# Optimization experiments

Hardware: AMD Instinct MI355X
Metric: run time of the kernel (lower is better)

The kernel has to match this reference:

```python
import jax, jax.numpy as jnp
import numpy as np

H = 16
D_MODEL = 1024
D_K = D_MODEL // H
B, S = 8, 1024


def setup_inputs() -> dict:
    key = jax.random.key(0)
    ks = jax.random.split(key, 11)
    scale = 1.0 / np.sqrt(D_MODEL)
    inp = {
        "query": jax.random.normal(ks[0], (B, S, D_MODEL), jnp.float32),
        "key_": jax.random.normal(ks[1], (B, S, D_MODEL), jnp.float32),
        "value": jax.random.normal(ks[2], (B, S, D_MODEL), jnp.float32),
        "w_q": jax.random.normal(ks[3], (D_MODEL, D_MODEL), jnp.float32) * scale,
        "b_q": jnp.zeros((D_MODEL,), jnp.float32),
        "w_k": jax.random.normal(ks[4], (D_MODEL, D_MODEL), jnp.float32) * scale,
        "b_k": jnp.zeros((D_MODEL,), jnp.float32),
        "w_v": jax.random.normal(ks[5], (D_MODEL, D_MODEL), jnp.float32) * scale,
        "b_v": jnp.zeros((D_MODEL,), jnp.float32),
        "w_o": jax.random.normal(ks[6], (D_MODEL, D_MODEL), jnp.float32) * scale,
        "b_o": jnp.zeros((D_MODEL,), jnp.float32),
    }
    return inp


def reference(query, key_, value, w_q, b_q, w_k, b_k, w_v, b_v, w_o, b_o):
    # Linear projections (torch Linear: x @ W.T + b), then split heads: [B,S,D] -> [B,H,S,d_k]
    def proj(x, w, b):
        y = jnp.einsum("bsd,ed->bse", x, w) + b
        return y.reshape(B, S, H, D_K).transpose(0, 2, 1, 3)

    q = proj(query, w_q, b_q)
    k = proj(key_, w_k, b_k)
    v = proj(value, w_v, b_v)

    # Scaled dot-product attention (mask=None, dropout p=0 -> identity)
    scores = jnp.einsum("bhqd,bhkd->bhqk", q, k) / jnp.sqrt(jnp.float32(D_K))
    attn = jax.nn.softmax(scores, axis=-1)
    ctx = jnp.einsum("bhqk,bhkd->bhqd", attn, v)  # [B,H,S,d_k]

    # Merge heads and final output projection
    ctx = ctx.transpose(0, 2, 1, 3).reshape(B, S, D_MODEL)
    return jnp.einsum("bsd,ed->bse", ctx, w_o) + b_o
```

## Files before the change

### kernel.cpp

```cpp
#include <hip/hip_runtime.h>
#include <hip/hip_bf16.h>

#define NH 16
#define DK 64
#define BB 8
#define SS 1024
#define DM 1024
#define MTOT (BB * SS)

typedef float f4v __attribute__((ext_vector_type(4)));
typedef float f16v __attribute__((ext_vector_type(16)));
typedef short s16v8 __attribute__((ext_vector_type(8)));
typedef unsigned short u16v4 __attribute__((ext_vector_type(4)));
typedef unsigned short u16v8 __attribute__((ext_vector_type(8)));

#define EXP2F(x) __builtin_amdgcn_exp2f(x)
#define WAIT_VM2() __builtin_amdgcn_s_waitcnt(0x0F72)
#define WAIT_VM0() __builtin_amdgcn_s_waitcnt(0x0F70)

__device__ __forceinline__ unsigned short f2bf(float x) {
    unsigned int u = __float_as_uint(x);
    u += 0x7FFFu + ((u >> 16) & 1u);
    return (unsigned short)(u >> 16);
}

__device__ __forceinline__ unsigned int packbf2(float lo, float hi) {
    return ((unsigned int)f2bf(hi) << 16) | f2bf(lo);
}

__device__ __forceinline__ void gload16(const void* g, void* l) {
    __builtin_amdgcn_global_load_lds(
        (const __attribute__((address_space(1))) void*)g,
        (__attribute__((address_space(3))) void*)l, 16, 0, 0);
}

struct Src7 { const float* p[7]; };

__global__ __launch_bounds__(256) void cvt_all(Src7 sp, unsigned short* __restrict__ dst) {
    const size_t e = ((size_t)blockIdx.x * 256 + threadIdx.x) * 8;
    const int unit = (int)(e >> 20);
    int t; size_t base;
    if (unit < 8)       { t = 0; base = 0; }
    else if (unit < 16) { t = 1; base = (size_t)8 << 20; }
    else if (unit < 24) { t = 2; base = (size_t)16 << 20; }
    else                { t = 3 + (unit - 24); base = (size_t)unit << 20; }
    const float* s = sp.p[t] + (e - base);
    f4v a = *(const f4v*)s;
    f4v b = *(const f4v*)(s + 4);
    u16v8 o;
    o[0] = f2bf(a[0]); o[1] = f2bf(a[1]); o[2] = f2bf(a[2]); o[3] = f2bf(a[3]);
    o[4] = f2bf(b[0]); o[5] = f2bf(b[1]); o[6] = f2bf(b[2]); o[7] = f2bf(b[3]);
    *(u16v8*)(dst + e) = o;
}

struct QkvArgs {
    const unsigned short* X[3];
    const unsigned short* W[3];
    const float* bias[3];
    unsigned short* Y[3];
};

__global__ __launch_bounds__(256) void gemm_qkv(QkvArgs a) {
    __shared__ unsigned short As[128 * 32];
    __shared__ unsigned short Bs[128 * 32];
    const int z = blockIdx.z;
    const unsigned short* X = a.X[z];
    const unsigned short* W = a.W[z];
    const float* bias = a.bias[z];
    unsigned short* Y = a.Y[z];

    const int tid = threadIdx.x;
    const int wv = tid >> 6, l = tid & 63;
    const int lq = l & 15, g = l >> 4;
    const int wr = wv >> 1, wc = wv & 1;
    const int m0 = blockIdx.x * 128, n0 = blockIdx.y * 128;

    f4v acc[4][4];
#pragma unroll
    for (int i = 0; i < 4; ++i)
#pragma unroll
        for (int j = 0; j < 4; ++j) acc[i][j] = (f4v){0.f, 0.f, 0.f, 0.f};

    for (int kt = 0; kt < DM / 32; ++kt) {
        const int k0 = kt * 32;
        __syncthreads();
#pragma unroll
        for (int p = 0; p < 2; ++p) {
            const int u = p * 256 + tid;
            const int row = u >> 2, kc = u & 3;
            gload16(X + (size_t)(m0 + row) * DM + k0 + kc * 8, As + (size_t)u * 8);
            gload16(W + (size_t)(n0 + row) * DM + k0 + kc * 8, Bs + (size_t)u * 8);
        }
        __syncthreads();

        s16v8 av[4], bv[4];
#pragma unroll
        for (int i = 0; i < 4; ++i)
            av[i] = *(const s16v8*)(As + (wr * 64 + i * 16 + lq) * 32 + g * 8);
#pragma unroll
        for (int j = 0; j < 4; ++j)
            bv[j] = *(const s16v8*)(Bs + (wc * 64 + j * 16 + lq) * 32 + g * 8);
#pragma unroll
        for (int i = 0; i < 4; ++i)
#pragma unroll
            for (int j = 0; j < 4; ++j)
                acc[i][j] = __builtin_amdgcn_mfma_f32_16x16x32_bf16(av[i], bv[j], acc[i][j], 0, 0, 0);
    }

#pragma unroll
    for (int j = 0; j < 4; ++j) {
        const int col = n0 + wc * 64 + j * 16 + lq;
        const float bvl = bias[col];
#pragma unroll
        for (int i = 0; i < 4; ++i) {
            const int row0 = m0 + wr * 64 + i * 16 + g * 4;
            if (z < 2) {
#pragma unroll
                for (int r = 0; r < 4; ++r) {
                    const int row = row0 + r;
                    const int b_ = row >> 10, s_ = row & (SS - 1);
                    const int h_ = col >> 6, d_ = col & (DK - 1);
                    Y[((size_t)(b_ * NH + h_) * SS + s_) * DK + d_] = f2bf(acc[i][j][r] + bvl);
                }
            } else {
                const int b_ = row0 >> 10, s0_ = row0 & (SS - 1);
                const int h_ = col >> 6, d_ = col & (DK - 1);
                u16v4 o;
#pragma unroll
                for (int r = 0; r < 4; ++r) o[r] = f2bf(acc[i][j][r] + bvl);
                *(u16v4*)&Y[((size_t)(b_ * NH + h_) * DK + d_) * SS + s0_] = o;
            }
        }
    }
}

__global__ __launch_bounds__(256) void gemm_out(const unsigned short* __restrict__ X,
                                                const unsigned short* __restrict__ W,
                                                const float* __restrict__ bias,
                                                float* __restrict__ Y) {
    __shared__ unsigned short As[128 * 32];
    __shared__ unsigned short Bs[128 * 32];
    const int tid = threadIdx.x;
    const int wv = tid >> 6, l = tid & 63;
    const int lq = l & 15, g = l >> 4;
    const int wr = wv >> 1, wc = wv & 1;
    const int m0 = blockIdx.x * 128, n0 = blockIdx.y * 128;

    f4v acc[4][4];
#pragma unroll
    for (int i = 0; i < 4; ++i)
#pragma unroll
        for (int j = 0; j < 4; ++j) acc[i][j] = (f4v){0.f, 0.f, 0.f, 0.f};

    for (int kt = 0; kt < DM / 32; ++kt) {
        const int k0 = kt * 32;
        __syncthreads();
#pragma unroll
        for (int p = 0; p < 2; ++p) {
            const int u = p * 256 + tid;
            const int row = u >> 2, kc = u & 3;
            gload16(X + (size_t)(m0 + row) * DM + k0 + kc * 8, As + (size_t)u * 8);
            gload16(W + (size_t)(n0 + row) * DM + k0 + kc * 8, Bs + (size_t)u * 8);
        }
        __syncthreads();

        s16v8 av[4], bv[4];
#pragma unroll
        for (int i = 0; i < 4; ++i)
            av[i] = *(const s16v8*)(As + (wr * 64 + i * 16 + lq) * 32 + g * 8);
#pragma unroll
        for (int j = 0; j < 4; ++j)
            bv[j] = *(const s16v8*)(Bs + (wc * 64 + j * 16 + lq) * 32 + g * 8);
#pragma unroll
        for (int i = 0; i < 4; ++i)
#pragma unroll
            for (int j = 0; j < 4; ++j)
                acc[i][j] = __builtin_amdgcn_mfma_f32_16x16x32_bf16(av[i], bv[j], acc[i][j], 0, 0, 0);
    }

#pragma unroll
    for (int j = 0; j < 4; ++j) {
        const int col = n0 + wc * 64 + j * 16 + lq;
        const float bvl = bias[col];
#pragma unroll
        for (int i = 0; i < 4; ++i) {
#pragma unroll
            for (int r = 0; r < 4; ++r) {
                const int row = m0 + wr * 64 + i * 16 + g * 4 + r;
                Y[(size_t)row * DM + col] = acc[i][j][r] + bvl;
            }
        }
    }
}

__global__ __launch_bounds__(512, 4) void attn_mfma32(const unsigned short* __restrict__ Qp,
                                                      const unsigned short* __restrict__ Kp,
                                                      const unsigned short* __restrict__ Vt,
                                                      unsigned short* __restrict__ ctx) {
    __shared__ unsigned short Sh[16384];
    const int tid = threadIdx.x;
    const int wv = tid >> 6;
    const int l = tid & 63;
    const int l31 = l & 31, hi = l >> 5;
    const int bh = blockIdx.x;
    const int qblk = blockIdx.y;
    const int q = qblk * 256 + wv * 32 + l31;
    const float C = 0.18033688011112042f;

#define ShK(buf) (Sh + (buf) * 4096)
#define ShV(buf) (Sh + 8192 + (buf) * 4096)

    const unsigned short* Qrow = Qp + ((size_t)bh * SS + q) * DK + hi * 8;
    s16v8 qf[4];
#pragma unroll
    for (int kd = 0; kd < 4; ++kd) qf[kd] = *(const s16v8*)(Qrow + kd * 16);

    const unsigned short* Kb = Kp + (size_t)bh * SS * DK;
    const unsigned short* Vb = Vt + (size_t)bh * DK * SS;

#define STAGE(buf, t)                                                       \
    {                                                                       \
        const int u = tid;                                                  \
        gload16(Kb + (size_t)((t) * 64 + (u & 63)) * DK + (u >> 6) * 8,     \
                ShK(buf) + (size_t)u * 8);                                  \
        gload16(Vb + (size_t)(u & 63) * SS + (t) * 64 + (u >> 6) * 8,       \
                ShV(buf) + (size_t)u * 8);                                  \
    }

    f16v O0, O1;
#pragma unroll
    for (int r = 0; r < 16; ++r) { O0[r] = 0.f; O1[r] = 0.f; }
    float me = -1e30f;
    float lr = 0.f;

    STAGE(0, 0);
    int cur = 0;

    for (int t = 0; t < SS / 64; ++t) {
        const int tn = (t < SS / 64 - 1) ? t + 1 : t;
        STAGE(cur ^ 1, tn);
        WAIT_VM2();
        __builtin_amdgcn_s_barrier();

        s16v8 kf[2][4];
#pragma unroll
        for (int ks = 0; ks < 2; ++ks)
#pragma unroll
            for (int kd = 0; kd < 4; ++kd)
                kf[ks][kd] = *(const s16v8*)(ShK(cur) + (((2 * kd + hi) * 64) + ks * 32 + l31) * 8);
        s16v8 vf[2][4];
#pragma unroll
        for (int db = 0; db < 2; ++db)
#pragma unroll
            for (int ksg = 0; ksg < 4; ++ksg)
                vf[db][ksg] = *(const s16v8*)(ShV(cur) + (((2 * ksg + hi) * 64) + db * 32 + l31) * 8);

        f16v s0, s1;
#pragma unroll
        for (int r = 0; r < 16; ++r) { s0[r] = 0.f; s1[r] = 0.f; }
#pragma unroll
        for (int kd = 0; kd < 4; ++kd) {
            s0 = __builtin_amdgcn_mfma_f32_32x32x16_bf16(kf[0][kd], qf[kd], s0, 0, 0, 0);
            s1 = __builtin_amdgcn_mfma_f32_32x32x16_bf16(kf[1][kd], qf[kd], s1, 0, 0, 0);
        }

        float mx = s0[0];
#pragma unroll
        for (int r = 1; r < 16; ++r) mx = fmaxf(mx, s0[r]);
#pragma unroll
        for (int r = 0; r < 16; ++r) mx = fmaxf(mx, s1[r]);
        mx = fmaxf(mx, __shfl_xor(mx, 32));
        const float mxl = mx * C;

        const bool need = !__all(mxl - me <= 8.0f);
        float corr = 1.0f;
        if (need) {
            const float mnew = fmaxf(me, mxl);
            corr = EXP2F(me - mnew);
            me = mnew;
        }

        float rs = 0.f;
#pragma unroll
        for (int r = 0; r < 16; ++r) { s0[r] = EXP2F(__fmaf_rn(s0[r], C, -me)); rs += s0[r]; }
#pragma unroll
        for (int r = 0; r < 16; ++r) { s1[r] = EXP2F(__fmaf_rn(s1[r], C, -me)); rs += s1[r]; }
        rs += __shfl_xor(rs, 32);
        if (need) {
            lr = lr * corr + rs;
#pragma unroll
            for (int r = 0; r < 16; ++r) { O0[r] *= corr; O1[r] *= corr; }
        } else {
            lr += rs;
        }

        s16v8 pb[2][2];
#pragma unroll
        for (int ks = 0; ks < 2; ++ks) {
            unsigned int u[8], su[8];
#pragma unroll
            for (int i = 0; i < 8; ++i) {
                const float plo = (ks == 0) ? s0[2 * i] : s1[2 * i];
                const float phi = (ks == 0) ? s0[2 * i + 1] : s1[2 * i + 1];
                u[i] = packbf2(plo, phi);
            }
#pragma unroll
            for (int i = 0; i < 8; ++i) su[i] = (unsigned int)__shfl_xor((int)u[i], 32);
#pragma unroll
            for (int kk = 0; kk < 2; ++kk) {
                const int base = 4 * kk + 2 * hi;
                union { unsigned int w[4]; s16v8 s; } f;
                f.w[0] = hi ? su[base] : u[base];
                f.w[1] = hi ? su[base + 1] : u[base + 1];
                f.w[2] = hi ? u[base] : su[base];
                f.w[3] = hi ? u[base + 1] : su[base + 1];
                pb[ks][kk] = f.s;
            }
        }

#pragma unroll
        for (int ksg = 0; ksg < 4; ++ksg) {
            O0 = __builtin_amdgcn_mfma_f32_32x32x16_bf16(vf[0][ksg], pb[ksg >> 1][ksg & 1], O0, 0, 0, 0);
            O1 = __builtin_amdgcn_mfma_f32_32x32x16_bf16(vf[1][ksg], pb[ksg >> 1][ksg & 1], O1, 0, 0, 0);
        }

        __builtin_amdgcn_s_barrier();
        cur ^= 1;
    }
#undef STAGE

    WAIT_VM0();
    __builtin_amdgcn_s_barrier();

    const float inv = 1.0f / lr;
    unsigned short* mybuf = Sh + wv * 2048;
#pragma unroll
    for (int db = 0; db < 2; ++db) {
        const f16v Ocur = db ? O1 : O0;
#pragma unroll
        for (int g2 = 0; g2 < 4; ++g2) {
            uint2 w;
            w.x = packbf2(Ocur[4 * g2 + 0] * inv, Ocur[4 * g2 + 1] * inv);
            w.y = packbf2(Ocur[4 * g2 + 2] * inv, Ocur[4 * g2 + 3] * inv);
            const int off = db * 64 + g2 * 16 + hi * 8;
            *(uint2*)((char*)mybuf + l31 * 128 + (off ^ ((l31 & 7) << 4))) = w;
        }
    }
    __syncthreads();

    const int r = l >> 1, h2 = l & 1;
    const int qrow = qblk * 256 + wv * 32 + r;
    const int b_ = bh >> 4, h_ = bh & 15;
    unsigned short* crow = ctx + ((size_t)b_ * SS + qrow) * DM + h_ * DK + h2 * 32;
#pragma unroll
    for (int j = 0; j < 4; ++j) {
        const int off = (h2 * 64 + j * 16) ^ ((r & 7) << 4);
        u16v8 v = *(const u16v8*)((const char*)mybuf + r * 128 + off);
        *(u16v8*)(crow + j * 8) = v;
    }
#undef ShK
#undef ShV
}

extern "C" void kernel_launch(void* const* d_in, const int* in_sizes, int n_in,
                              void* d_out, int out_size, void* d_ws, size_t ws_size,
                              hipStream_t stream) {
    const float* query = (const float*)d_in[0];
    const float* key_  = (const float*)d_in[1];
    const float* value = (const float*)d_in[2];
    const float* w_q = (const float*)d_in[3];
    const float* b_q = (const float*)d_in[4];
    const float* w_k = (const float*)d_in[5];
    const float* b_k = (const float*)d_in[6];
    const float* w_v = (const float*)d_in[7];
    const float* b_v = (const float*)d_in[8];
    const float* w_o = (const float*)d_in[9];
    const float* b_o = (const float*)d_in[10];

    unsigned short* ws = (unsigned short*)d_ws;
    const size_t NX = (size_t)MTOT * DM;
    const size_t NW = (size_t)DM * DM;
    unsigned short* xq  = ws;
    unsigned short* xk  = xq + NX;
    unsigned short* xv  = xk + NX;
    unsigned short* wqb = xv + NX;
    unsigned short* wkb = wqb + NW;
    unsigned short* wvb = wkb + NW;
    unsigned short* wob = wvb + NW;
    unsigned short* Qp  = wob + NW;
    unsigned short* Kp  = Qp + NX;
    unsigned short* VpT = Kp + NX;
    unsigned short* ctx = xq;

    Src7 sp;
    sp.p[0] = query; sp.p[1] = key_; sp.p[2] = value;
    sp.p[3] = w_q; sp.p[4] = w_k; sp.p[5] = w_v; sp.p[6] = w_o;
    cvt_all<<<14336, 256, 0, stream>>>(sp, ws);

    QkvArgs qa;
    qa.X[0] = xq;  qa.X[1] = xk;  qa.X[2] = xv;
    qa.W[0] = wqb; qa.W[1] = wkb; qa.W[2] = wvb;
    qa.bias[0] = b_q; qa.bias[1] = b_k; qa.bias[2] = b_v;
    qa.Y[0] = Qp; qa.Y[1] = Kp; qa.Y[2] = VpT;
    gemm_qkv<<<dim3(MTOT / 128, DM / 128, 3), 256, 0, stream>>>(qa);

    attn_mfma32<<<dim3(BB * NH, SS / 256), 512, 0, stream>>>(Qp, Kp, VpT, ctx);

    gemm_out<<<dim3(MTOT / 128, DM / 128), 256, 0, stream>>>(ctx, wob, b_o, (float*)d_out);
}
```

Before: 362.9 us.

## Shrink attention blocks to 4 waves, defer V loads, interleave softmax packing

```diff
diff --git a/kernel.cpp b/kernel.cpp
--- a/kernel.cpp
+++ b/kernel.cpp
@@ -15,7 +15,7 @@
 typedef unsigned short u16v8 __attribute__((ext_vector_type(8)));
 
 #define EXP2F(x) __builtin_amdgcn_exp2f(x)
-#define WAIT_VM2() __builtin_amdgcn_s_waitcnt(0x0F72)
+#define WAIT_VM4() __builtin_amdgcn_s_waitcnt(0x0F74)
 #define WAIT_VM0() __builtin_amdgcn_s_waitcnt(0x0F70)
 
 __device__ __forceinline__ unsigned short f2bf(float x) {
@@ -25,7 +25,10 @@
 }
 
 __device__ __forceinline__ unsigned int packbf2(float lo, float hi) {
-    return ((unsigned int)f2bf(hi) << 16) | f2bf(lo);
+    __hip_bfloat162 b = __float22bfloat162_rn(make_float2(lo, hi));
+    union { __hip_bfloat162 b; unsigned int u; } c;
+    c.b = b;
+    return c.u;
 }
 
 __device__ __forceinline__ void gload16(const void* g, void* l) {
@@ -193,22 +196,20 @@
     }
 }
 
-__global__ __launch_bounds__(512, 4) void attn_mfma32(const unsigned short* __restrict__ Qp,
+__global__ __launch_bounds__(256, 3) void attn_mfma32(const unsigned short* __restrict__ Qp,
                                                       const unsigned short* __restrict__ Kp,
                                                       const unsigned short* __restrict__ Vt,
                                                       unsigned short* __restrict__ ctx) {
-    __shared__ unsigned short Sh[16384];
+    __shared__ unsigned short Ksh[2][4096];
+    __shared__ unsigned short Vsh[2][4096];
     const int tid = threadIdx.x;
     const int wv = tid >> 6;
     const int l = tid & 63;
     const int l31 = l & 31, hi = l >> 5;
     const int bh = blockIdx.x;
     const int qblk = blockIdx.y;
-    const int q = qblk * 256 + wv * 32 + l31;
+    const int q = qblk * 128 + wv * 32 + l31;
     const float C = 0.18033688011112042f;
-
-#define ShK(buf) (Sh + (buf) * 4096)
-#define ShV(buf) (Sh + 8192 + (buf) * 4096)
 
     const unsigned short* Qrow = Qp + ((size_t)bh * SS + q) * DK + hi * 8;
     s16v8 qf[4];
@@ -218,13 +219,15 @@
     const unsigned short* Kb = Kp + (size_t)bh * SS * DK;
     const unsigned short* Vb = Vt + (size_t)bh * DK * SS;
 
-#define STAGE(buf, t)                                                       \
-    {                                                                       \
-        const int u = tid;                                                  \
-        gload16(Kb + (size_t)((t) * 64 + (u & 63)) * DK + (u >> 6) * 8,     \
-                ShK(buf) + (size_t)u * 8);                                  \
-        gload16(Vb + (size_t)(u & 63) * SS + (t) * 64 + (u >> 6) * 8,       \
-                ShV(buf) + (size_t)u * 8);                                  \
+#define STAGE(buf, t)                                                            \
+    {                                                                            \
+        _Pragma("unroll") for (int p = 0; p < 2; ++p) {                          \
+            const int u = p * 256 + tid;                                         \
+            gload16(Kb + (size_t)((t) * 64 + (u & 63)) * DK + (u >> 6) * 8,      \
+                    &Ksh[buf][(size_t)u * 8]);                                   \
+            gload16(Vb + (size_t)(u & 63) * SS + (t) * 64 + (u >> 6) * 8,        \
+                    &Vsh[buf][(size_t)u * 8]);                                   \
+        }                                                                        \
     }
 
     f16v O0, O1;
@@ -239,7 +242,7 @@
     for (int t = 0; t < SS / 64; ++t) {
         const int tn = (t < SS / 64 - 1) ? t + 1 : t;
         STAGE(cur ^ 1, tn);
-        WAIT_VM2();
+        WAIT_VM4();
         __builtin_amdgcn_s_barrier();
 
         s16v8 kf[2][4];
@@ -247,13 +250,7 @@
         for (int ks = 0; ks < 2; ++ks)
 #pragma unroll
             for (int kd = 0; kd < 4; ++kd)
-                kf[ks][kd] = *(const s16v8*)(ShK(cur) + (((2 * kd + hi) * 64) + ks * 32 + l31) * 8);
-        s16v8 vf[2][4];
-#pragma unroll
-        for (int db = 0; db < 2; ++db)
-#pragma unroll
-            for (int ksg = 0; ksg < 4; ++ksg)
-                vf[db][ksg] = *(const s16v8*)(ShV(cur) + (((2 * ksg + hi) * 64) + db * 32 + l31) * 8);
+                kf[ks][kd] = *(const s16v8*)&Ksh[cur][(((2 * kd + hi) * 64) + ks * 32 + l31) * 8];
 
         f16v s0, s1;
 #pragma unroll
@@ -281,29 +278,13 @@
         }
 
         float rs = 0.f;
+        s16v8 pb[2][2];
 #pragma unroll
         for (int r = 0; r < 16; ++r) { s0[r] = EXP2F(__fmaf_rn(s0[r], C, -me)); rs += s0[r]; }
-#pragma unroll
-        for (int r = 0; r < 16; ++r) { s1[r] = EXP2F(__fmaf_rn(s1[r], C, -me)); rs += s1[r]; }
-        rs += __shfl_xor(rs, 32);
-        if (need) {
-            lr = lr * corr + rs;
-#pragma unroll
-            for (int r = 0; r < 16; ++r) { O0[r] *= corr; O1[r] *= corr; }
-        } else {
-            lr += rs;
-        }
-
-        s16v8 pb[2][2];
-#pragma unroll
-        for (int ks = 0; ks < 2; ++ks) {
+        {
             unsigned int u[8], su[8];
 #pragma unroll
-            for (int i = 0; i < 8; ++i) {
-                const float plo = (ks == 0) ? s0[2 * i] : s1[2 * i];
-                const float phi = (ks == 0) ? s0[2 * i + 1] : s1[2 * i + 1];
-                u[i] = packbf2(plo, phi);
-            }
+            for (int i = 0; i < 8; ++i) u[i] = packbf2(s0[2 * i], s0[2 * i + 1]);
 #pragma unroll
             for (int i = 0; i < 8; ++i) su[i] = (unsigned int)__shfl_xor((int)u[i], 32);
 #pragma unroll
@@ -314,14 +295,44 @@
                 f.w[1] = hi ? su[base + 1] : u[base + 1];
                 f.w[2] = hi ? u[base] : su[base];
                 f.w[3] = hi ? u[base + 1] : su[base + 1];
-                pb[ks][kk] = f.s;
+                pb[0][kk] = f.s;
             }
         }
+#pragma unroll
+        for (int r = 0; r < 16; ++r) { s1[r] = EXP2F(__fmaf_rn(s1[r], C, -me)); rs += s1[r]; }
+        {
+            unsigned int u[8], su[8];
+#pragma unroll
+            for (int i = 0; i < 8; ++i) u[i] = packbf2(s1[2 * i], s1[2 * i + 1]);
+#pragma unroll
+            for (int i = 0; i < 8; ++i) su[i] = (unsigned int)__shfl_xor((int)u[i], 32);
+#pragma unroll
+            for (int kk = 0; kk < 2; ++kk) {
+                const int base = 4 * kk + 2 * hi;
+                union { unsigned int w[4]; s16v8 s; } f;
+                f.w[0] = hi ? su[base] : u[base];
+                f.w[1] = hi ? su[base + 1] : u[base + 1];
+                f.w[2] = hi ? u[base] : su[base];
+                f.w[3] = hi ? u[base + 1] : su[base + 1];
+                pb[1][kk] = f.s;
+            }
+        }
+
+        rs += __shfl_xor(rs, 32);
+        if (need) {
+            lr = lr * corr + rs;
+#pragma unroll
+            for (int r = 0; r < 16; ++r) { O0[r] *= corr; O1[r] *= corr; }
+        } else {
+            lr += rs;
+        }
 
 #pragma unroll
         for (int ksg = 0; ksg < 4; ++ksg) {
-            O0 = __builtin_amdgcn_mfma_f32_32x32x16_bf16(vf[0][ksg], pb[ksg >> 1][ksg & 1], O0, 0, 0, 0);
-            O1 = __builtin_amdgcn_mfma_f32_32x32x16_bf16(vf[1][ksg], pb[ksg >> 1][ksg & 1], O1, 0, 0, 0);
+            s16v8 vf0 = *(const s16v8*)&Vsh[cur][(((2 * ksg + hi) * 64) + l31) * 8];
+            s16v8 vf1 = *(const s16v8*)&Vsh[cur][(((2 * ksg + hi) * 64) + 32 + l31) * 8];
+            O0 = __builtin_amdgcn_mfma_f32_32x32x16_bf16(vf0, pb[ksg >> 1][ksg & 1], O0, 0, 0, 0);
+            O1 = __builtin_amdgcn_mfma_f32_32x32x16_bf16(vf1, pb[ksg >> 1][ksg & 1], O1, 0, 0, 0);
         }
 
         __builtin_amdgcn_s_barrier();
@@ -333,7 +344,7 @@
     __builtin_amdgcn_s_barrier();
 
     const float inv = 1.0f / lr;
-    unsigned short* mybuf = Sh + wv * 2048;
+    unsigned short* mybuf = &Ksh[0][0] + wv * 2048;
 #pragma unroll
     for (int db = 0; db < 2; ++db) {
         const f16v Ocur = db ? O1 : O0;
@@ -349,7 +360,7 @@
     __syncthreads();
 
     const int r = l >> 1, h2 = l & 1;
-    const int qrow = qblk * 256 + wv * 32 + r;
+    const int qrow = qblk * 128 + wv * 32 + r;
     const int b_ = bh >> 4, h_ = bh & 15;
     unsigned short* crow = ctx + ((size_t)b_ * SS + qrow) * DM + h_ * DK + h2 * 32;
 #pragma unroll
@@ -358,8 +369,6 @@
         u16v8 v = *(const u16v8*)((const char*)mybuf + r * 128 + off);
         *(u16v8*)(crow + j * 8) = v;
     }
-#undef ShK
-#undef ShV
 }
 
 extern "C" void kernel_launch(void* const* d_in, const int* in_sizes, int n_in,
@@ -404,7 +413,7 @@
     qa.Y[0] = Qp; qa.Y[1] = Kp; qa.Y[2] = VpT;
     gemm_qkv<<<dim3(MTOT / 128, DM / 128, 3), 256, 0, stream>>>(qa);
 
-    attn_mfma32<<<dim3(BB * NH, SS / 256), 512, 0, stream>>>(Qp, Kp, VpT, ctx);
+    attn_mfma32<<<dim3(BB * NH, SS / 128), 256, 0, stream>>>(Qp, Kp, VpT, ctx);
 
     gemm_out<<<dim3(MTOT / 128, DM / 128), 256, 0, stream>>>(ctx, wob, b_o, (float*)d_out);
 }
```

After: 373.9 us. 3.0% more time.
